# Optimization experiments

Measured on AMD Instinct MI355X. Metric: run time of the kernel, lower is better.

The kernel has to match this reference:

```python
import jax, jax.numpy as jnp
import numpy as np

B = 4096
N_DENSE = 13
N_SPARSE = 26
VOCAB = 100000
EMB = 8
CIN_SIZE = [26, 128, 128]


def setup_inputs() -> dict:
    key = jax.random.key(0)
    ks = jax.random.split(key, 24)
    s = 0.05
    dense = jax.random.normal(ks[0], (B, N_DENSE), dtype=jnp.float32)
    sparse = jax.random.randint(ks[1], (B, N_SPARSE), 0, VOCAB).astype(jnp.float32)
    inputs = jnp.concatenate([dense, sparse], axis=1)  # [B, 39]
    emb_tables = jax.random.normal(ks[2], (N_SPARSE, VOCAB, EMB), dtype=jnp.float32) * s
    linear_W = jax.random.normal(ks[3], (39, 1), dtype=jnp.float32) * s
    linear_b = jnp.zeros((1,), dtype=jnp.float32)
    # CIN Conv3d weights: kernel (H_prev, H0, 1) with out_channels H_next -> [H_next, H_prev, H0]
    W_cin0 = jax.random.normal(ks[4], (CIN_SIZE[1], CIN_SIZE[0], CIN_SIZE[0]), dtype=jnp.float32) * s
    b_cin0 = jnp.zeros((CIN_SIZE[1],), dtype=jnp.float32)
    W_cin1 = jax.random.normal(ks[5], (CIN_SIZE[2], CIN_SIZE[1], CIN_SIZE[0]), dtype=jnp.float32) * s
    b_cin1 = jnp.zeros((CIN_SIZE[2],), dtype=jnp.float32)
    cin_lin_W = jax.random.normal(ks[6], (256, 1), dtype=jnp.float32) * s
    cin_lin_b = jnp.zeros((1,), dtype=jnp.float32)
    d_W1 = jax.random.normal(ks[7], (221, 256), dtype=jnp.float32) * s
    d_b1 = jnp.zeros((256,), dtype=jnp.float32)
    d_W2 = jax.random.normal(ks[8], (256, 128), dtype=jnp.float32) * s
    d_b2 = jnp.zeros((128,), dtype=jnp.float32)
    d_W3 = jax.random.normal(ks[9], (128, 64), dtype=jnp.float32) * s
    d_b3 = jnp.zeros((64,), dtype=jnp.float32)
    d_W4 = jax.random.normal(ks[10], (64, 1), dtype=jnp.float32) * s
    d_b4 = jnp.zeros((1,), dtype=jnp.float32)
    return dict(inputs=inputs, emb_tables=emb_tables, linear_W=linear_W, linear_b=linear_b,
                W_cin0=W_cin0, b_cin0=b_cin0, W_cin1=W_cin1, b_cin1=b_cin1,
                cin_lin_W=cin_lin_W, cin_lin_b=cin_lin_b,
                d_W1=d_W1, d_b1=d_b1, d_W2=d_W2, d_b2=d_b2,
                d_W3=d_W3, d_b3=d_b3, d_W4=d_W4, d_b4=d_b4)


def reference(inputs, emb_tables, linear_W, linear_b,
              W_cin0, b_cin0, W_cin1, b_cin1, cin_lin_W, cin_lin_b,
              d_W1, d_b1, d_W2, d_b2, d_W3, d_b3, d_W4, d_b4):
    dense_in = inputs[:, :N_DENSE]                       # [B, 13]
    sparse_idx = inputs[:, N_DENSE:].astype(jnp.int32)   # [B, 26]

    # linear part over the raw inputs
    linear_out = inputs @ linear_W + linear_b            # [B, 1]

    # per-field embedding lookup: tables [F, V, E], idx [B, F] -> emb [B, F, E]
    emb = jax.vmap(lambda t, i: t[i], in_axes=(0, 1), out_axes=1)(emb_tables, sparse_idx)

    # CIN: each layer is an outer product over fields followed by a full-extent
    # Conv3d, i.e. X_{l+1}[b,o,k] = sum_{i,j} X_l[b,i,k] * X_0[b,j,k] * W[o,i,j] + b[o]
    X0 = emb
    Xi = emb
    res = []
    for W, b in ((W_cin0, b_cin0), (W_cin1, b_cin1)):
        Xi = jnp.einsum('bik,bjk,oij->bok', Xi, X0, W) + b[None, :, None]
        res.append(Xi)
    cin_feat = jnp.sum(jnp.concatenate(res, axis=1), axis=-1)  # [B, 256]
    cin_out = jax.nn.relu(cin_feat @ cin_lin_W + cin_lin_b)    # [B, 1]

    # dense MLP over [dense | flattened embeddings]
    h = jnp.concatenate([dense_in, emb.reshape(emb.shape[0], -1)], axis=1)  # [B, 221]
    h = jax.nn.relu(h @ d_W1 + d_b1)
    h = jax.nn.relu(h @ d_W2 + d_b2)
    h = jax.nn.relu(h @ d_W3 + d_b3)
    dense_out = jax.nn.relu(h @ d_W4 + d_b4)                   # [B, 1]

    return jax.nn.sigmoid(linear_out + cin_out + dense_out).reshape(-1)  # [B]
```

## Files before the change

kernel.cpp:

```cpp
#include <hip/hip_runtime.h>
#include <math.h>

#define B     4096
#define ND    13
#define NS    26
#define NF    39
#define VOCAB 100000
#define NP    351
#define NPP   360
#define CHP   45
#define GSTR  28
#define RPB   8
#define TPB   512
#define XSS   212

#define OFF_GST 0
#define OFF_CST 10080
#define OFF_C2J 10088
#define OFF_LUT 10120

__global__ __launch_bounds__(256) void k_pre(const float* __restrict__ W0,
                                             const float* __restrict__ W1,
                                             const float* __restrict__ b0,
                                             const float* __restrict__ b1,
                                             const float* __restrict__ clw,
                                             float* __restrict__ Gst,
                                             float* __restrict__ cst,
                                             float* __restrict__ c2j,
                                             int* __restrict__ lutg) {
    int blk = blockIdx.x, tid = threadIdx.x;
    if (blk < 26) {
        int j = blk;
        __shared__ float vh[2][128];
        __shared__ float vj[128];
        __shared__ float c2r[2];
        {
            int i = tid & 127, h = tid >> 7;
            const float* wp = W1 + (long)(h * 64) * 3328 + i * 26 + j;
            float acc = 0.f;
#pragma unroll 8
            for (int o = 0; o < 64; o++) acc += clw[128 + h * 64 + o] * wp[o * 3328];
            vh[h][i] = acc;
        }
        __syncthreads();
        if (tid < 128) {
            float vv = vh[0][tid] + vh[1][tid];
            vj[tid] = vv;
            float c = vv * b0[tid];
            for (int off = 32; off; off >>= 1) c += __shfl_down(c, off, 64);
            if ((tid & 63) == 0) c2r[tid >> 6] = c;
        }
        __syncthreads();
        if (tid == 0) c2j[j] = c2r[0] + c2r[1];
        for (int p = tid; p < NPP; p += 256) {
            float g = 0.f;
            if (p < NP) {
                int l = 0, rem = p;
                while (rem >= NS - l) { rem -= NS - l; l++; }
                int m = l + rem;
                float sym = (l != m) ? 1.f : 0.f;
                const float* wa = W0 + l * 26 + m;
                const float* wb = W0 + m * 26 + l;
#pragma unroll 8
                for (int i = 0; i < 128; i++)
                    g += vj[i] * (wa[i * 676] + sym * wb[i * 676]);
            }
            Gst[p * GSTR + j] = g;
        }
    } else if (blk == 26) {
        for (int p = tid; p < NPP; p += 256) {
            float a = 0.f; int lmbits = 0;
            if (p < NP) {
                int l = 0, rem = p;
                while (rem >= NS - l) { rem -= NS - l; l++; }
                int m = l + rem;
                float sym = (l != m) ? 1.f : 0.f;
                const float* wa = W0 + l * 26 + m;
                const float* wb = W0 + m * 26 + l;
#pragma unroll 8
                for (int o = 0; o < 128; o++)
                    a += clw[o] * (wa[o * 676] + sym * wb[o * 676]);
                lmbits = (l << 5) | m;
            }
            Gst[p * GSTR + 26] = a;
            Gst[p * GSTR + 27] = __int_as_float(lmbits);
            lutg[p] = lmbits;
        }
    } else {
        __shared__ float red[2];
        float c = 0.f;
        if (tid < 128) {
            c = clw[tid] * b0[tid] + clw[128 + tid] * b1[tid];
            for (int off = 32; off; off >>= 1) c += __shfl_down(c, off, 64);
            if ((tid & 63) == 0) red[tid >> 6] = c;
        }
        __syncthreads();
        if (tid == 0) cst[0] = 8.f * (red[0] + red[1]);
    }
}

__global__ __launch_bounds__(512, 4) void k_main(
    const float* __restrict__ inputs, const float* __restrict__ tables,
    const float* __restrict__ lW, const float* __restrict__ lb,
    const float* __restrict__ Gst, const float* __restrict__ c2j,
    const float* __restrict__ cst, const int* __restrict__ lutg,
    const float* __restrict__ dW1, const float* __restrict__ db1,
    const float* __restrict__ dW2, const float* __restrict__ db2,
    const float* __restrict__ dW3, const float* __restrict__ db3,
    const float* __restrict__ dW4, const float* __restrict__ db4,
    const float* __restrict__ clb,
    float* __restrict__ out) {
    __shared__ float xs[RPB][XSS];
    __shared__ float inTf[221 * 8];
    __shared__ float h1Tf[256 * 12];
    __shared__ float4 pbuf4[1024];
    __shared__ float lin_s[RPB];
    __shared__ float redbuf[4][RPB];

    float* h2Tf = inTf;
    float* pbufF = (float*)pbuf4;

    int tid = threadIdx.x;
    int b0r = blockIdx.x * RPB;

    if (tid < 416) {
        int r = tid / 52, t2 = tid - r * 52;
        int f = t2 >> 1, hf = t2 & 1;
        int idx = (int)inputs[(b0r + r) * NF + ND + f];
        const float4* src = (const float4*)(tables + ((long)f * VOCAB + idx) * 8);
        *(float4*)&xs[r][f * 8 + hf * 4] = src[hf];
    }
    if (tid >= 448 && tid < 448 + RPB) {
        int r = tid - 448;
        float acc = lb[0];
        for (int c = 0; c < NF; c++) acc += inputs[(b0r + r) * NF + c] * lW[c];
        lin_s[r] = acc;
    }
    __syncthreads();

    for (int e = tid; e < 221 * 8; e += TPB) {
        int c = e >> 3, r = e & 7;
        inTf[c * 8 + r] = (c < ND) ? inputs[(b0r + r) * NF + c] : xs[r][c - ND];
    }
    __syncthreads();

    {
        int w = tid >> 6;
        int wu = __builtin_amdgcn_readfirstlane(w);
        int lane = tid & 63;
        if (wu < 4) {
            int row = lane >> 3, k = lane & 7;
            const float* xrow = &xs[row][0];
            float t[27];
#pragma unroll
            for (int j = 0; j < 27; j++) t[j] = 0.f;
#pragma unroll 1
            for (int half = 0; half < 2; half++) {
                int ch = 2 * wu + half;
                const float4* g4 = (const float4*)Gst + ch * CHP * 7;
                const int* lu = lutg + ch * CHP;
#pragma unroll 5
                for (int pi = 0; pi < CHP; pi++) {
                    int lm = lu[pi];
                    float q = xrow[(lm >> 5) * 8 + k] * xrow[(lm & 31) * 8 + k];
                    float4 g0 = g4[pi * 7 + 0], g1 = g4[pi * 7 + 1];
                    float4 g2 = g4[pi * 7 + 2], g3 = g4[pi * 7 + 3];
                    float4 g4v = g4[pi * 7 + 4], g5 = g4[pi * 7 + 5];
                    float4 g6 = g4[pi * 7 + 6];
                    t[0]  += g0.x * q; t[1]  += g0.y * q; t[2]  += g0.z * q; t[3]  += g0.w * q;
                    t[4]  += g1.x * q; t[5]  += g1.y * q; t[6]  += g1.z * q; t[7]  += g1.w * q;
                    t[8]  += g2.x * q; t[9]  += g2.y * q; t[10] += g2.z * q; t[11] += g2.w * q;
                    t[12] += g3.x * q; t[13] += g3.y * q; t[14] += g3.z * q; t[15] += g3.w * q;
                    t[16] += g4v.x * q; t[17] += g4v.y * q; t[18] += g4v.z * q; t[19] += g4v.w * q;
                    t[20] += g5.x * q; t[21] += g5.y * q; t[22] += g5.z * q; t[23] += g5.w * q;
                    t[24] += g6.x * q; t[25] += g6.y * q; t[26] += g6.z * q;
                }
            }
            float csel = (wu == 0) ? 1.f : 0.f;
            float part = t[26];
#pragma unroll
            for (int j = 0; j < 26; j++) {
                float xv = xrow[j * 8 + k];
                part += (t[j] + csel * c2j[j]) * xv;
            }
            part += __shfl_xor(part, 1, 64);
            part += __shfl_xor(part, 2, 64);
            part += __shfl_xor(part, 4, 64);
            if (k == 0) redbuf[wu][row] = part;
        } else {
            int o = tid & 255;
            float4 S0 = make_float4(0.f, 0.f, 0.f, 0.f);
            float4 S1 = S0;
#pragma unroll 4
            for (int c = 0; c < 221; c++) {
                float wv = dW1[c * 256 + o];
                float4 i0 = *(const float4*)&inTf[c * 8];
                float4 i1 = *(const float4*)&inTf[c * 8 + 4];
                S0.x += i0.x * wv; S0.y += i0.y * wv; S0.z += i0.z * wv; S0.w += i0.w * wv;
                S1.x += i1.x * wv; S1.y += i1.y * wv; S1.z += i1.z * wv; S1.w += i1.w * wv;
            }
            float bb = db1[o];
            S0.x = fmaxf(S0.x + bb, 0.f); S0.y = fmaxf(S0.y + bb, 0.f);
            S0.z = fmaxf(S0.z + bb, 0.f); S0.w = fmaxf(S0.w + bb, 0.f);
            S1.x = fmaxf(S1.x + bb, 0.f); S1.y = fmaxf(S1.y + bb, 0.f);
            S1.z = fmaxf(S1.z + bb, 0.f); S1.w = fmaxf(S1.w + bb, 0.f);
            *(float4*)&h1Tf[o * 12]     = S0;
            *(float4*)&h1Tf[o * 12 + 4] = S1;
        }
    }
    __syncthreads();

    {
        int o = tid & 127, cg = tid >> 7;
        int c0 = cg << 6;
        float4 A0 = make_float4(0.f, 0.f, 0.f, 0.f);
        float4 A1 = A0;
#pragma unroll 4
        for (int cc = 0; cc < 64; cc++) {
            int c = c0 + cc;
            float wv = dW2[c * 128 + o];
            float4 i0 = *(const float4*)&h1Tf[c * 12];
            float4 i1 = *(const float4*)&h1Tf[c * 12 + 4];
            A0.x += i0.x * wv; A0.y += i0.y * wv; A0.z += i0.z * wv; A0.w += i0.w * wv;
            A1.x += i1.x * wv; A1.y += i1.y * wv; A1.z += i1.z * wv; A1.w += i1.w * wv;
        }
        int pb = (cg * 128 + o) * 2;
        pbuf4[pb]     = A0;
        pbuf4[pb + 1] = A1;
    }
    __syncthreads();

    if (tid < 128) {
        int o = tid;
        float bb = db2[o];
        float sx0 = bb, sy0 = bb, sz0 = bb, sw0 = bb;
        float sx1 = bb, sy1 = bb, sz1 = bb, sw1 = bb;
#pragma unroll
        for (int cg = 0; cg < 4; cg++) {
            float4 p0 = pbuf4[(cg * 128 + o) * 2];
            float4 p1 = pbuf4[(cg * 128 + o) * 2 + 1];
            sx0 += p0.x; sy0 += p0.y; sz0 += p0.z; sw0 += p0.w;
            sx1 += p1.x; sy1 += p1.y; sz1 += p1.z; sw1 += p1.w;
        }
        float4 S0, S1;
        S0.x = fmaxf(sx0, 0.f); S0.y = fmaxf(sy0, 0.f);
        S0.z = fmaxf(sz0, 0.f); S0.w = fmaxf(sw0, 0.f);
        S1.x = fmaxf(sx1, 0.f); S1.y = fmaxf(sy1, 0.f);
        S1.z = fmaxf(sz1, 0.f); S1.w = fmaxf(sw1, 0.f);
        *(float4*)&h2Tf[o * 12]     = S0;
        *(float4*)&h2Tf[o * 12 + 4] = S1;
    }
    __syncthreads();

    {
        int o = tid & 63, cg = tid >> 6;
        int c0 = cg << 4;
        float4 A0 = make_float4(0.f, 0.f, 0.f, 0.f);
        float4 A1 = A0;
#pragma unroll 8
        for (int cc = 0; cc < 16; cc++) {
            int c = c0 + cc;
            float wv = dW3[c * 64 + o];
            float4 i0 = *(const float4*)&h2Tf[c * 12];
            float4 i1 = *(const float4*)&h2Tf[c * 12 + 4];
            A0.x += i0.x * wv; A0.y += i0.y * wv; A0.z += i0.z * wv; A0.w += i0.w * wv;
            A1.x += i1.x * wv; A1.y += i1.y * wv; A1.z += i1.z * wv; A1.w += i1.w * wv;
        }
        int pb = (cg * 64 + o) * 2;
        pbuf4[pb]     = A0;
        pbuf4[pb + 1] = A1;
    }
    __syncthreads();

    {
        int r = tid >> 6, o = tid & 63;
        float s = 0.f;
#pragma unroll
        for (int cg = 0; cg < 8; cg++)
            s += pbufF[(cg * 64 + o) * 8 + r];
        float h3 = fmaxf(s + db3[o], 0.f) * dW4[o];
        h3 += __shfl_xor(h3, 1, 64);
        h3 += __shfl_xor(h3, 2, 64);
        h3 += __shfl_xor(h3, 4, 64);
        h3 += __shfl_xor(h3, 8, 64);
        h3 += __shfl_xor(h3, 16, 64);
        h3 += __shfl_xor(h3, 32, 64);
        if (o == 0) {
            float scin = cst[0];
#pragma unroll
            for (int w = 0; w < 4; w++) scin += redbuf[w][r];
            float dense = fmaxf(h3 + db4[0], 0.f);
            float cin = fmaxf(scin + clb[0], 0.f);
            float x = lin_s[r] + cin + dense;
            out[b0r + r] = 1.f / (1.f + expf(-x));
        }
    }
}

extern "C" void kernel_launch(void* const* d_in, const int* in_sizes, int n_in,
                              void* d_out, int out_size, void* d_ws, size_t ws_size,
                              hipStream_t stream) {
    const float* inputs = (const float*)d_in[0];
    const float* tables = (const float*)d_in[1];
    const float* lW     = (const float*)d_in[2];
    const float* lb     = (const float*)d_in[3];
    const float* W0     = (const float*)d_in[4];
    const float* b0     = (const float*)d_in[5];
    const float* W1c    = (const float*)d_in[6];
    const float* b1c    = (const float*)d_in[7];
    const float* clw    = (const float*)d_in[8];
    const float* clb    = (const float*)d_in[9];
    const float* dW1    = (const float*)d_in[10];
    const float* db1    = (const float*)d_in[11];
    const float* dW2    = (const float*)d_in[12];
    const float* db2    = (const float*)d_in[13];
    const float* dW3    = (const float*)d_in[14];
    const float* db3    = (const float*)d_in[15];
    const float* dW4    = (const float*)d_in[16];
    const float* db4    = (const float*)d_in[17];

    float* ws   = (float*)d_ws;
    float* Gst  = ws + OFF_GST;
    float* cst  = ws + OFF_CST;
    float* c2j  = ws + OFF_C2J;
    int*   lutg = (int*)(ws + OFF_LUT);

    k_pre<<<28, 256, 0, stream>>>(W0, W1c, b0, b1c, clw, Gst, cst, c2j, lutg);
    k_main<<<B / RPB, TPB, 0, stream>>>(inputs, tables, lW, lb, Gst, c2j, cst, lutg,
                                        dW1, db1, dW2, db2, dW3, db3, dW4, db4, clb,
                                        (float*)d_out);
}
```

Measured before the change: 222.6 us.

## Run CIN on all eight waves then MLP on all, dropping partial-sum buffers

The CIN pair loop is now spread over all 8 waves instead of 4 waves doing two chunks each, and the first MLP layer runs afterwards on all 512 threads, each covering 4 rows. Later MLP layers split rows across thread groups rather than splitting the reduction dimension, which removes the pbuf partial-sum buffer, its reduction pass and its extra barriers. The embedding gather writes the transposed MLP input directly, removing one transpose pass and one sync, and the pair index is read from the packed Gst slot so the separate lutg table goes away. In exchange, CIN and MLP no longer run concurrently on different waves, and each weight load now feeds fewer FMAs.

```diff
diff --git a/kernel.cpp b/kernel.cpp
--- a/kernel.cpp
+++ b/kernel.cpp
@@ -17,7 +17,6 @@
 #define OFF_GST 0
 #define OFF_CST 10080
 #define OFF_C2J 10088
-#define OFF_LUT 10120
 
 __global__ __launch_bounds__(256) void k_pre(const float* __restrict__ W0,
                                              const float* __restrict__ W1,
@@ -26,8 +25,7 @@
                                              const float* __restrict__ clw,
                                              float* __restrict__ Gst,
                                              float* __restrict__ cst,
-                                             float* __restrict__ c2j,
-                                             int* __restrict__ lutg) {
+                                             float* __restrict__ c2j) {
     int blk = blockIdx.x, tid = threadIdx.x;
     if (blk < 26) {
         int j = blk;
@@ -84,7 +82,6 @@
             }
             Gst[p * GSTR + 26] = a;
             Gst[p * GSTR + 27] = __int_as_float(lmbits);
-            lutg[p] = lmbits;
         }
     } else {
         __shared__ float red[2];
@@ -103,7 +100,7 @@
     const float* __restrict__ inputs, const float* __restrict__ tables,
     const float* __restrict__ lW, const float* __restrict__ lb,
     const float* __restrict__ Gst, const float* __restrict__ c2j,
-    const float* __restrict__ cst, const int* __restrict__ lutg,
+    const float* __restrict__ cst,
     const float* __restrict__ dW1, const float* __restrict__ db1,
     const float* __restrict__ dW2, const float* __restrict__ db2,
     const float* __restrict__ dW3, const float* __restrict__ db3,
@@ -113,172 +110,123 @@
     __shared__ float xs[RPB][XSS];
     __shared__ float inTf[221 * 8];
     __shared__ float h1Tf[256 * 12];
-    __shared__ float4 pbuf4[1024];
     __shared__ float lin_s[RPB];
-    __shared__ float redbuf[4][RPB];
+    __shared__ float redbuf[8][RPB];
 
     float* h2Tf = inTf;
-    float* pbufF = (float*)pbuf4;
 
     int tid = threadIdx.x;
     int b0r = blockIdx.x * RPB;
 
-    if (tid < 416) {
-        int r = tid / 52, t2 = tid - r * 52;
-        int f = t2 >> 1, hf = t2 & 1;
+    if (tid < RPB * NS) {
+        int r = tid / NS, f = tid - r * NS;
         int idx = (int)inputs[(b0r + r) * NF + ND + f];
         const float4* src = (const float4*)(tables + ((long)f * VOCAB + idx) * 8);
-        *(float4*)&xs[r][f * 8 + hf * 4] = src[hf];
-    }
-    if (tid >= 448 && tid < 448 + RPB) {
-        int r = tid - 448;
+        float4 a = src[0], b4 = src[1];
+        *(float4*)&xs[r][f * 8] = a;
+        *(float4*)&xs[r][f * 8 + 4] = b4;
+        int cb = (ND + f * 8) * 8 + r;
+        inTf[cb]      = a.x;  inTf[cb + 8]   = a.y;
+        inTf[cb + 16] = a.z;  inTf[cb + 24]  = a.w;
+        inTf[cb + 32] = b4.x; inTf[cb + 40]  = b4.y;
+        inTf[cb + 48] = b4.z; inTf[cb + 56]  = b4.w;
+    } else if (tid < 208 + ND * RPB) {
+        int t = tid - 208;
+        int c = t >> 3, r = t & 7;
+        inTf[c * 8 + r] = inputs[(b0r + r) * NF + c];
+    }
+    if (tid >= 496 && tid < 496 + RPB) {
+        int r = tid - 496;
         float acc = lb[0];
         for (int c = 0; c < NF; c++) acc += inputs[(b0r + r) * NF + c] * lW[c];
         lin_s[r] = acc;
     }
     __syncthreads();
 
-    for (int e = tid; e < 221 * 8; e += TPB) {
-        int c = e >> 3, r = e & 7;
-        inTf[c * 8 + r] = (c < ND) ? inputs[(b0r + r) * NF + c] : xs[r][c - ND];
-    }
-    __syncthreads();
-
     {
         int w = tid >> 6;
         int wu = __builtin_amdgcn_readfirstlane(w);
         int lane = tid & 63;
-        if (wu < 4) {
-            int row = lane >> 3, k = lane & 7;
-            const float* xrow = &xs[row][0];
-            float t[27];
+        int row = lane >> 3, k = lane & 7;
+        const float4* g4 = (const float4*)Gst + wu * CHP * 7;
+        const float* xrow = &xs[row][0];
+        float csel = (wu == 0) ? 1.f : 0.f;
+        float t[27];
 #pragma unroll
-            for (int j = 0; j < 27; j++) t[j] = 0.f;
-#pragma unroll 1
-            for (int half = 0; half < 2; half++) {
-                int ch = 2 * wu + half;
-                const float4* g4 = (const float4*)Gst + ch * CHP * 7;
-                const int* lu = lutg + ch * CHP;
-#pragma unroll 5
-                for (int pi = 0; pi < CHP; pi++) {
-                    int lm = lu[pi];
-                    float q = xrow[(lm >> 5) * 8 + k] * xrow[(lm & 31) * 8 + k];
-                    float4 g0 = g4[pi * 7 + 0], g1 = g4[pi * 7 + 1];
-                    float4 g2 = g4[pi * 7 + 2], g3 = g4[pi * 7 + 3];
-                    float4 g4v = g4[pi * 7 + 4], g5 = g4[pi * 7 + 5];
-                    float4 g6 = g4[pi * 7 + 6];
-                    t[0]  += g0.x * q; t[1]  += g0.y * q; t[2]  += g0.z * q; t[3]  += g0.w * q;
-                    t[4]  += g1.x * q; t[5]  += g1.y * q; t[6]  += g1.z * q; t[7]  += g1.w * q;
-                    t[8]  += g2.x * q; t[9]  += g2.y * q; t[10] += g2.z * q; t[11] += g2.w * q;
-                    t[12] += g3.x * q; t[13] += g3.y * q; t[14] += g3.z * q; t[15] += g3.w * q;
-                    t[16] += g4v.x * q; t[17] += g4v.y * q; t[18] += g4v.z * q; t[19] += g4v.w * q;
-                    t[20] += g5.x * q; t[21] += g5.y * q; t[22] += g5.z * q; t[23] += g5.w * q;
-                    t[24] += g6.x * q; t[25] += g6.y * q; t[26] += g6.z * q;
-                }
-            }
-            float csel = (wu == 0) ? 1.f : 0.f;
-            float part = t[26];
+        for (int j = 0; j < 27; j++) t[j] = 0.f;
+#pragma unroll 3
+        for (int pi = 0; pi < CHP; pi++) {
+            float4 g6 = g4[pi * 7 + 6];
+            int lm = __float_as_int(g6.w);
+            float q = xrow[(lm >> 5) * 8 + k] * xrow[(lm & 31) * 8 + k];
+            float4 g0 = g4[pi * 7 + 0], g1 = g4[pi * 7 + 1];
+            float4 g2 = g4[pi * 7 + 2], g3 = g4[pi * 7 + 3];
+            float4 g4v = g4[pi * 7 + 4], g5 = g4[pi * 7 + 5];
+            t[0]  += g0.x * q; t[1]  += g0.y * q; t[2]  += g0.z * q; t[3]  += g0.w * q;
+            t[4]  += g1.x * q; t[5]  += g1.y * q; t[6]  += g1.z * q; t[7]  += g1.w * q;
+            t[8]  += g2.x * q; t[9]  += g2.y * q; t[10] += g2.z * q; t[11] += g2.w * q;
+            t[12] += g3.x * q; t[13] += g3.y * q; t[14] += g3.z * q; t[15] += g3.w * q;
+            t[16] += g4v.x * q; t[17] += g4v.y * q; t[18] += g4v.z * q; t[19] += g4v.w * q;
+            t[20] += g5.x * q; t[21] += g5.y * q; t[22] += g5.z * q; t[23] += g5.w * q;
+            t[24] += g6.x * q; t[25] += g6.y * q; t[26] += g6.z * q;
+        }
+        float part = t[26];
 #pragma unroll
-            for (int j = 0; j < 26; j++) {
-                float xv = xrow[j * 8 + k];
-                part += (t[j] + csel * c2j[j]) * xv;
-            }
-            part += __shfl_xor(part, 1, 64);
-            part += __shfl_xor(part, 2, 64);
-            part += __shfl_xor(part, 4, 64);
-            if (k == 0) redbuf[wu][row] = part;
-        } else {
-            int o = tid & 255;
-            float4 S0 = make_float4(0.f, 0.f, 0.f, 0.f);
-            float4 S1 = S0;
+        for (int j = 0; j < 26; j++) {
+            float xv = xrow[j * 8 + k];
+            part += (t[j] + csel * c2j[j]) * xv;
+        }
+        part += __shfl_xor(part, 1, 64);
+        part += __shfl_xor(part, 2, 64);
+        part += __shfl_xor(part, 4, 64);
+        if (k == 0) redbuf[w][row] = part;
+    }
+
+    {
+        int o = tid & 255, g = tid >> 8;
+        const float* ip = inTf + 4 * g;
+        float4 A = make_float4(0.f, 0.f, 0.f, 0.f);
 #pragma unroll 4
-            for (int c = 0; c < 221; c++) {
-                float wv = dW1[c * 256 + o];
-                float4 i0 = *(const float4*)&inTf[c * 8];
-                float4 i1 = *(const float4*)&inTf[c * 8 + 4];
-                S0.x += i0.x * wv; S0.y += i0.y * wv; S0.z += i0.z * wv; S0.w += i0.w * wv;
-                S1.x += i1.x * wv; S1.y += i1.y * wv; S1.z += i1.z * wv; S1.w += i1.w * wv;
-            }
-            float bb = db1[o];
-            S0.x = fmaxf(S0.x + bb, 0.f); S0.y = fmaxf(S0.y + bb, 0.f);
-            S0.z = fmaxf(S0.z + bb, 0.f); S0.w = fmaxf(S0.w + bb, 0.f);
-            S1.x = fmaxf(S1.x + bb, 0.f); S1.y = fmaxf(S1.y + bb, 0.f);
-            S1.z = fmaxf(S1.z + bb, 0.f); S1.w = fmaxf(S1.w + bb, 0.f);
-            *(float4*)&h1Tf[o * 12]     = S0;
-            *(float4*)&h1Tf[o * 12 + 4] = S1;
-        }
+        for (int c = 0; c < 221; c++) {
+            float wv = dW1[c * 256 + o];
+            float4 iv = *(const float4*)&ip[c * 8];
+            A.x += iv.x * wv; A.y += iv.y * wv; A.z += iv.z * wv; A.w += iv.w * wv;
+        }
+        float bb = db1[o];
+        float4 S;
+        S.x = fmaxf(A.x + bb, 0.f); S.y = fmaxf(A.y + bb, 0.f);
+        S.z = fmaxf(A.z + bb, 0.f); S.w = fmaxf(A.w + bb, 0.f);
+        *(float4*)&h1Tf[o * 12 + 4 * g] = S;
     }
     __syncthreads();
 
     {
-        int o = tid & 127, cg = tid >> 7;
-        int c0 = cg << 6;
-        float4 A0 = make_float4(0.f, 0.f, 0.f, 0.f);
-        float4 A1 = A0;
+        int o = tid & 127, g = tid >> 7;
+        const float* ip = h1Tf + 2 * g;
+        float a0 = 0.f, a1 = 0.f;
 #pragma unroll 4
-        for (int cc = 0; cc < 64; cc++) {
-            int c = c0 + cc;
+        for (int c = 0; c < 256; c++) {
             float wv = dW2[c * 128 + o];
-            float4 i0 = *(const float4*)&h1Tf[c * 12];
-            float4 i1 = *(const float4*)&h1Tf[c * 12 + 4];
-            A0.x += i0.x * wv; A0.y += i0.y * wv; A0.z += i0.z * wv; A0.w += i0.w * wv;
-            A1.x += i1.x * wv; A1.y += i1.y * wv; A1.z += i1.z * wv; A1.w += i1.w * wv;
-        }
-        int pb = (cg * 128 + o) * 2;
-        pbuf4[pb]     = A0;
-        pbuf4[pb + 1] = A1;
+            float2 iv = *(const float2*)&ip[c * 12];
+            a0 += iv.x * wv; a1 += iv.y * wv;
+        }
+        float bb = db2[o];
+        a0 = fmaxf(a0 + bb, 0.f); a1 = fmaxf(a1 + bb, 0.f);
+        h2Tf[o * 12 + 2 * g]     = a0;
+        h2Tf[o * 12 + 2 * g + 1] = a1;
     }
     __syncthreads();
 
-    if (tid < 128) {
-        int o = tid;
-        float bb = db2[o];
-        float sx0 = bb, sy0 = bb, sz0 = bb, sw0 = bb;
-        float sx1 = bb, sy1 = bb, sz1 = bb, sw1 = bb;
-#pragma unroll
-        for (int cg = 0; cg < 4; cg++) {
-            float4 p0 = pbuf4[(cg * 128 + o) * 2];
-            float4 p1 = pbuf4[(cg * 128 + o) * 2 + 1];
-            sx0 += p0.x; sy0 += p0.y; sz0 += p0.z; sw0 += p0.w;
-            sx1 += p1.x; sy1 += p1.y; sz1 += p1.z; sw1 += p1.w;
-        }
-        float4 S0, S1;
-        S0.x = fmaxf(sx0, 0.f); S0.y = fmaxf(sy0, 0.f);
-        S0.z = fmaxf(sz0, 0.f); S0.w = fmaxf(sw0, 0.f);
-        S1.x = fmaxf(sx1, 0.f); S1.y = fmaxf(sy1, 0.f);
-        S1.z = fmaxf(sz1, 0.f); S1.w = fmaxf(sw1, 0.f);
-        *(float4*)&h2Tf[o * 12]     = S0;
-        *(float4*)&h2Tf[o * 12 + 4] = S1;
-    }
-    __syncthreads();
-
-    {
-        int o = tid & 63, cg = tid >> 6;
-        int c0 = cg << 4;
-        float4 A0 = make_float4(0.f, 0.f, 0.f, 0.f);
-        float4 A1 = A0;
-#pragma unroll 8
-        for (int cc = 0; cc < 16; cc++) {
-            int c = c0 + cc;
+    {
+        int o = tid & 63, g = tid >> 6;
+        float acc = 0.f;
+#pragma unroll 4
+        for (int c = 0; c < 128; c++) {
             float wv = dW3[c * 64 + o];
-            float4 i0 = *(const float4*)&h2Tf[c * 12];
-            float4 i1 = *(const float4*)&h2Tf[c * 12 + 4];
-            A0.x += i0.x * wv; A0.y += i0.y * wv; A0.z += i0.z * wv; A0.w += i0.w * wv;
-            A1.x += i1.x * wv; A1.y += i1.y * wv; A1.z += i1.z * wv; A1.w += i1.w * wv;
-        }
-        int pb = (cg * 64 + o) * 2;
-        pbuf4[pb]     = A0;
-        pbuf4[pb + 1] = A1;
-    }
-    __syncthreads();
-
-    {
-        int r = tid >> 6, o = tid & 63;
-        float s = 0.f;
-#pragma unroll
-        for (int cg = 0; cg < 8; cg++)
-            s += pbufF[(cg * 64 + o) * 8 + r];
-        float h3 = fmaxf(s + db3[o], 0.f) * dW4[o];
+            float hv = h2Tf[c * 12 + g];
+            acc += hv * wv;
+        }
+        float h3 = fmaxf(acc + db3[o], 0.f) * dW4[o];
         h3 += __shfl_xor(h3, 1, 64);
         h3 += __shfl_xor(h3, 2, 64);
         h3 += __shfl_xor(h3, 4, 64);
@@ -288,11 +236,11 @@
         if (o == 0) {
             float scin = cst[0];
 #pragma unroll
-            for (int w = 0; w < 4; w++) scin += redbuf[w][r];
+            for (int w2 = 0; w2 < 8; w2++) scin += redbuf[w2][g];
             float dense = fmaxf(h3 + db4[0], 0.f);
             float cin = fmaxf(scin + clb[0], 0.f);
-            float x = lin_s[r] + cin + dense;
-            out[b0r + r] = 1.f / (1.f + expf(-x));
+            float x = lin_s[g] + cin + dense;
+            out[b0r + g] = 1.f / (1.f + expf(-x));
         }
     }
 }
@@ -323,10 +271,9 @@
     float* Gst  = ws + OFF_GST;
     float* cst  = ws + OFF_CST;
     float* c2j  = ws + OFF_C2J;
-    int*   lutg = (int*)(ws + OFF_LUT);
-
-    k_pre<<<28, 256, 0, stream>>>(W0, W1c, b0, b1c, clw, Gst, cst, c2j, lutg);
-    k_main<<<B / RPB, TPB, 0, stream>>>(inputs, tables, lW, lb, Gst, c2j, cst, lutg,
+
+    k_pre<<<28, 256, 0, stream>>>(W0, W1c, b0, b1c, clw, Gst, cst, c2j);
+    k_main<<<B / RPB, TPB, 0, stream>>>(inputs, tables, lW, lb, Gst, c2j, cst,
                                         dW1, db1, dW2, db2, dW3, db3, dW4, db4, clb,
                                         (float*)d_out);
 }
```

Result: slower. 248.1 us (+11.4%).
